# Kernel optimization log

Measured on AMD Instinct MI355X. Metric: run time of the kernel, lower is better.

The kernel has to match this reference:

```python
import jax, jax.numpy as jnp
import numpy as np
import math

RES = 320
DECIMATION = 4
M = RES * RES // DECIMATION  # 25600 trajectory points
OVERSAMP = 1.25
WIDTH = 4
BETA = math.pi * (((WIDTH / OVERSAMP) * (OVERSAMP - 0.5)) ** 2 - 0.8) ** 0.5
B = 16


def setup_inputs() -> dict:
    key = jax.random.key(0)
    k1, k2 = jax.random.split(key)
    k_space_input = jax.random.normal(k1, (B, 1, RES, RES, 2), dtype=jnp.float32)
    # learnable k-space trajectory, coords in [-RES/2, RES/2)
    trajectory = (jax.random.uniform(k2, (M, 2), dtype=jnp.float32) - 0.5) * RES
    return {"k_space_input": k_space_input, "trajectory": trajectory}


def _grid_sample_bilinear(img, traj):
    # img: [B, C, H, W]; traj: [M, 2] = (x, y) in [-res/2, res/2]
    # Matches torch grid_sample(align_corners=True, padding_mode='zeros')
    # after normalizing traj by (res/2).
    Bn, C, H, W = img.shape
    gx = traj[:, 0] / (W / 2)
    gy = traj[:, 1] / (H / 2)
    px = (gx + 1.0) * 0.5 * (W - 1)
    py = (gy + 1.0) * 0.5 * (H - 1)
    x0 = jnp.floor(px)
    y0 = jnp.floor(py)
    wx1 = px - x0
    wy1 = py - y0
    out = jnp.zeros((Bn, C, traj.shape[0]), img.dtype)
    for dy in (0, 1):
        for dx in (0, 1):
            xi = x0 + dx
            yi = y0 + dy
            w = (wx1 if dx else 1.0 - wx1) * (wy1 if dy else 1.0 - wy1)
            inb = (xi >= 0) & (xi < W) & (yi >= 0) & (yi < H)
            xc = jnp.clip(xi, 0, W - 1).astype(jnp.int32)
            yc = jnp.clip(yi, 0, H - 1).astype(jnp.int32)
            out = out + img[:, :, yc, xc] * (w * inb)[None, None, :]
    return out  # [B, C, M]


def _kb_weight(delta, half):
    # Kaiser-Bessel interpolation kernel (sigpy convention, 1/width factor per dim)
    x = delta / half
    t = jnp.maximum(1.0 - x * x, 0.0)
    return jnp.i0(BETA * jnp.sqrt(t)) / WIDTH


def _nufft_adjoint(y, coord, H, W):
    # y: [B, M] complex64; coord: [M,2], coord[:,0]->H axis, coord[:,1]->W axis
    osH = math.ceil(OVERSAMP * H)
    osW = math.ceil(OVERSAMP * W)
    scale = jnp.array([osH / H, osW / W], jnp.float32)
    shift = jnp.array([osH // 2, osW // 2], jnp.float32)
    c = coord * scale + shift  # scaled to oversampled-grid coords
    half = WIDTH / 2.0
    start = jnp.ceil(c - half)                       # [M,2]
    offs = jnp.arange(WIDTH, dtype=jnp.float32)
    idx = start[:, :, None] + offs                   # [M,2,WIDTH]
    w = _kb_weight(c[:, :, None] - idx, half)        # [M,2,WIDTH]
    iy = idx[:, 0].astype(jnp.int32) % osH           # [M,WIDTH]
    ix = idx[:, 1].astype(jnp.int32) % osW
    ww = w[:, 0, :, None] * w[:, 1, None, :]         # [M,WIDTH,WIDTH]
    flat = (iy[:, :, None] * osW + ix[:, None, :]).reshape(-1)  # [M*WIDTH^2]
    Bn = y.shape[0]
    contrib = (y[:, :, None, None] * ww[None]).reshape(Bn, -1)  # [B, M*WIDTH^2]
    grid = jnp.zeros((Bn, osH * osW), y.dtype).at[:, flat].add(contrib)
    grid = grid.reshape(Bn, osH, osW)
    # centered unnormalized-to-ortho IFFT (sigpy scaling)
    img = jnp.fft.fftshift(
        jnp.fft.ifft2(jnp.fft.ifftshift(grid, axes=(-2, -1)), axes=(-2, -1)),
        axes=(-2, -1))
    img = img * ((osH * osW) / math.sqrt(H * W))
    sy = osH // 2 - H // 2
    sx = osW // 2 - W // 2
    img = img[:, sy:sy + H, sx:sx + W]  # center crop

    def apod(n, os_n):
        a = jnp.sqrt(jnp.maximum(
            BETA ** 2 - (np.pi * WIDTH * (jnp.arange(n, dtype=jnp.float32) - n // 2) / os_n) ** 2,
            1e-12))
        return a / jnp.sinh(a)

    img = img * apod(H, osH)[:, None] * apod(W, osW)[None, :]
    return img  # [B, H, W] complex


def reference(k_space_input, trajectory):
    # [B,1,H,W,2] -> [B,2,H,W] (real/imag channels)
    ksp = jnp.transpose(k_space_input, (0, 1, 4, 2, 3))[:, 0]
    sub = _grid_sample_bilinear(ksp, trajectory)          # [B,2,M]
    y = (sub[:, 0] + 1j * sub[:, 1]).astype(jnp.complex64)
    img = _nufft_adjoint(y, trajectory, ksp.shape[-2], ksp.shape[-1])
    out = jnp.stack([img.real, img.imag], axis=1)          # [B,2,H,W]
    return out[:, None]                                    # [B,1,2,H,W]
```

## Files before the change

kernel.cpp:

```cpp
#include <hip/hip_runtime.h>

#define NPTS   25600
#define NB     16
#define NRES   320
#define OS     400
#define NCELL  (OS * OS)
#define CAP    16
#define MAXOVF 4096

#define NJ     8
#define FFTTH  512
#define LSTRV  404

#define BETA_F (3.14159265358979f * 2.22710574513201f)

__device__ __forceinline__ float bessel_i0f(float x) {
    float ax = fabsf(x);
    if (ax < 3.75f) {
        float t = (ax * ax) * (1.0f / 14.0625f);
        return 1.0f + t * (3.5156229f + t * (3.0899424f + t * (1.2067492f +
                     t * (0.2659732f + t * (0.0360768f + t * 0.0045813f)))));
    } else {
        float t = 3.75f / ax;
        return (expf(ax) * rsqrtf(ax)) *
               (0.39894228f + t * (0.01328592f + t * (0.00225319f + t * (-0.00157565f +
                t * (0.00916281f + t * (-0.02057706f + t * (0.02635537f +
                t * (-0.01647633f + t * 0.00392377f))))))));
    }
}

struct OvfEntry { int cell; int m; float w; float pad; };

__global__ __launch_bounds__(256)
void k_sample_taps(const float* __restrict__ ksp,
                   const float* __restrict__ traj,
                   float2* __restrict__ val,
                   int* __restrict__ cursor,
                   float2* __restrict__ entries,
                   int* __restrict__ ovf_cnt,
                   OvfEntry* __restrict__ ovf)
{
    int blk = blockIdx.x;
    if (blk < 1600) {
        int gid = blk * 256 + threadIdx.x;
        int b = gid & 15;
        int m = gid >> 4;

        float tx = traj[2 * m + 0];
        float ty = traj[2 * m + 1];

        float px = (tx * (1.0f / 160.0f) + 1.0f) * 0.5f * 319.0f;
        float py = (ty * (1.0f / 160.0f) + 1.0f) * 0.5f * 319.0f;
        float fx0 = floorf(px), fy0 = floorf(py);
        int x0 = (int)fx0, y0 = (int)fy0;
        float wx1 = px - fx0, wy1 = py - fy0;
        float wx0 = 1.0f - wx1, wy0 = 1.0f - wy1;
        x0 = min(max(x0, 0), NRES - 1);
        y0 = min(max(y0, 0), NRES - 1);
        int x1 = min(x0 + 1, NRES - 1);
        int y1 = min(y0 + 1, NRES - 1);

        const float2* base = (const float2*)ksp + (size_t)b * NRES * NRES;
        float2 v00 = base[y0 * NRES + x0];
        float2 v01 = base[y0 * NRES + x1];
        float2 v10 = base[y1 * NRES + x0];
        float2 v11 = base[y1 * NRES + x1];
        float sr = (v00.x * wx0 + v01.x * wx1) * wy0 + (v10.x * wx0 + v11.x * wx1) * wy1;
        float si = (v00.y * wx0 + v01.y * wx1) * wy0 + (v10.y * wx0 + v11.y * wx1) * wy1;

        val[gid] = make_float2(sr, si);
    } else {
        int m = (blk - 1600) * 256 + threadIdx.x;
        if (m >= NPTS) return;

        float tx = traj[2 * m + 0];
        float ty = traj[2 * m + 1];
        float c0 = tx * 1.25f + 200.0f;
        float c1 = ty * 1.25f + 200.0f;
        float s0 = ceilf(c0 - 2.0f);
        float s1 = ceilf(c1 - 2.0f);

        float w0[4], w1[4];
        int   i0[4], i1[4];
#pragma unroll
        for (int t = 0; t < 4; t++) {
            float id0 = s0 + (float)t;
            float d0 = (c0 - id0) * 0.5f;
            float t0 = fmaxf(1.0f - d0 * d0, 0.0f);
            w0[t] = bessel_i0f(BETA_F * sqrtf(t0)) * 0.25f;
            i0[t] = (((int)id0) + OS) % OS;

            float id1 = s1 + (float)t;
            float d1 = (c1 - id1) * 0.5f;
            float t1 = fmaxf(1.0f - d1 * d1, 0.0f);
            w1[t] = bessel_i0f(BETA_F * sqrtf(t1)) * 0.25f;
            i1[t] = (((int)id1) + OS) % OS;
        }

#pragma unroll
        for (int t0 = 0; t0 < 4; t0++) {
#pragma unroll
            for (int t1 = 0; t1 < 4; t1++) {
                int cell = i1[t1] * OS + i0[t0];
                float w = w0[t0] * w1[t1];
                int slot = atomicAdd(&cursor[cell], 1);
                if (slot < CAP) {
                    entries[(size_t)slot * NCELL + cell] = make_float2(__int_as_float(m), w);
                } else {
                    int oi = atomicAdd(ovf_cnt, 1);
                    if (oi < MAXOVF) { ovf[oi].cell = cell; ovf[oi].m = m; ovf[oi].w = w; }
                }
            }
        }
    }
}

__global__ __launch_bounds__(256)
void k_gather(const int* __restrict__ cursor,
              const float2* __restrict__ entries,
              const float4* __restrict__ val4,
              float2* __restrict__ grid,
              const int* __restrict__ ovf_cnt,
              const OvfEntry* __restrict__ ovf)
{
    int cell = blockIdx.x * blockDim.x + threadIdx.x;
    if (cell >= NCELL) return;
    int cnt_raw = cursor[cell];
    int cnt = min(cnt_raw, CAP);

    float4 acc[8];
#pragma unroll
    for (int q = 0; q < 8; q++) acc[q] = make_float4(0.f, 0.f, 0.f, 0.f);

    for (int k = 0; k < cnt; k++) {
        float2 e = entries[(size_t)k * NCELL + cell];
        int m = __float_as_int(e.x);
        float w = e.y;
        const float4* v = val4 + (size_t)m * 8;
#pragma unroll
        for (int q = 0; q < 8; q++) {
            float4 x = v[q];
            acc[q].x = fmaf(w, x.x, acc[q].x);
            acc[q].y = fmaf(w, x.y, acc[q].y);
            acc[q].z = fmaf(w, x.z, acc[q].z);
            acc[q].w = fmaf(w, x.w, acc[q].w);
        }
    }

    if (cnt_raw > CAP) {
        int n = min(*ovf_cnt, MAXOVF);
        for (int i = 0; i < n; i++) {
            if (ovf[i].cell != cell) continue;
            int m = ovf[i].m;
            float w = ovf[i].w;
            const float4* v = val4 + (size_t)m * 8;
#pragma unroll
            for (int q = 0; q < 8; q++) {
                float4 x = v[q];
                acc[q].x = fmaf(w, x.x, acc[q].x);
                acc[q].y = fmaf(w, x.y, acc[q].y);
                acc[q].z = fmaf(w, x.z, acc[q].z);
                acc[q].w = fmaf(w, x.w, acc[q].w);
            }
        }
    }

#pragma unroll
    for (int q = 0; q < 8; q++) {
        grid[(size_t)(2 * q + 0) * NCELL + cell] = make_float2(acc[q].x, acc[q].y);
        grid[(size_t)(2 * q + 1) * NCELL + cell] = make_float2(acc[q].z, acc[q].w);
    }
}


__device__ __forceinline__ float apodf(int i) {
    float t = (float)(i - 160) * 0.031415926535897932f;
    float a = sqrtf(fmaxf(BETA_F * BETA_F - t * t, 1e-12f));
    return a / sinhf(a);
}

__global__ __launch_bounds__(FFTTH)
void k_fft_pass_a(const float* __restrict__ grid, float* __restrict__ At)
{
    __shared__ float2 A[NJ * LSTRV];
    __shared__ float4 B4[NJ * 200];
    __shared__ float2 E20t[20];
    __shared__ float2 E400p[424];
    int tid = threadIdx.x;
    int b = blockIdx.y;
    int j0 = blockIdx.x * NJ;

    for (int t = tid; t < 400; t += FFTTH) {
        float sn, cs;
        sincosf((float)t * 0.015707963267948966f, &sn, &cs);
        E400p[t + (t >> 4)] = make_float2(cs, sn);
    }
    if (tid < 20) {
        float sn, cs;
        sincosf((float)tid * 0.3141592653589793f, &sn, &cs);
        E20t[tid] = make_float2(cs, sn);
    }
    const float4* g4 = (const float4*)(grid + ((size_t)b * NCELL + (size_t)j0 * OS) * 2);
    for (int o = tid; o < NJ * 200; o += FFTTH) {
        int r = o / 200, q = o - r * 200;
        *((float4*)&A[r * LSTRV] + q) = g4[r * 200 + q];
    }
    __syncthreads();

    for (int o = tid; o < NJ * 200; o += FFTTH) {
        int r = o / 200, rem = o - r * 200;
        int j = rem / 20, n2 = rem - j * 20;
        const float2* Al = &A[r * LSTRV];
        float4 outv;
        if (j == 0) {
            float2 a0 = Al[n2], a1 = Al[n2 + 200];
            outv = make_float4(a0.x, a0.y, a1.x, a1.y);
        } else {
            float2 a0 = Al[n2 + 20 * j], a1 = Al[n2 + 20 * (20 - j)];
            outv = make_float4(a0.x + a1.x, a0.y + a1.y, a0.x - a1.x, a0.y - a1.y);
        }
        B4[r * 200 + j * 20 + n2] = outv;
    }
    __syncthreads();

    for (int o = tid; o < NJ * 200; o += FFTTH) {
        int r = o / 200, rem = o - r * 200;
        int k1h = rem / 20, n2 = rem - k1h * 20;
        const float4* Bl = &B4[r * 200];
        float4 b0 = Bl[n2];
        float2* Ar_ = &A[r * LSTRV + 20 * n2];
        if (k1h == 0) {
            float b_r = b0.x + b0.z, b_i = b0.y + b0.w;
            float a0r = 0.f, a0i = 0.f, d0r = 0.f, d0i = 0.f;
#pragma unroll
            for (int j = 1; j <= 9; j++) {
                float4 P = Bl[j * 20 + n2];
                a0r += P.x; a0i += P.y;
                float sg = (j & 1) ? -1.f : 1.f;
                d0r = fmaf(sg, P.x, d0r); d0i = fmaf(sg, P.y, d0i);
            }
            Ar_[0] = make_float2(b_r + a0r, b_i + a0i);
            int ti = 10 * n2;
            float2 tw = E400p[ti + (ti >> 4)];
            float xr = b_r + d0r, xi = b_i + d0i;
            Ar_[10] = make_float2(xr * tw.x - xi * tw.y, xr * tw.y + xi * tw.x);
        } else {
            float sgn = (k1h & 1) ? -1.f : 1.f;
            float b_r = fmaf(sgn, b0.z, b0.x), b_i = fmaf(sgn, b0.w, b0.y);
            float2 ek = E20t[k1h];
            float c = ek.x, s = ek.y;
            float Asr = 0.f, Asi = 0.f, Bsr = 0.f, Bsi = 0.f;
#pragma unroll
            for (int j = 1; j <= 9; j++) {
                float4 P = Bl[j * 20 + n2];
                Asr = fmaf(c, P.x, Asr); Asi = fmaf(c, P.y, Asi);
                Bsr = fmaf(s, P.w, Bsr); Bsi = fmaf(s, P.z, Bsi);
                float cn = c * ek.x - s * ek.y;
                s = c * ek.y + s * ek.x;
                c = cn;
            }
            float x1r = b_r + Asr - Bsr, x1i = b_i + Asi + Bsi;
            float x2r = b_r + Asr + Bsr, x2i = b_i + Asi - Bsi;
            int t1 = n2 * k1h;
            int t2 = n2 * (20 - k1h);
            float2 tw1 = E400p[t1 + (t1 >> 4)];
            float2 tw2 = E400p[t2 + (t2 >> 4)];
            Ar_[k1h]      = make_float2(x1r * tw1.x - x1i * tw1.y, x1r * tw1.y + x1i * tw1.x);
            Ar_[20 - k1h] = make_float2(x2r * tw2.x - x2i * tw2.y, x2r * tw2.y + x2i * tw2.x);
        }
    }
    __syncthreads();

    for (int o = tid; o < NJ * 200; o += FFTTH) {
        int r = o / 200, rem = o - r * 200;
        int j = rem / 20, k1 = rem - j * 20;
        const float2* Sl = &A[r * LSTRV];
        float4 outv;
        if (j == 0) {
            float2 a0 = Sl[k1], a1 = Sl[200 + k1];
            outv = make_float4(a0.x, a0.y, a1.x, a1.y);
        } else {
            float2 a0 = Sl[20 * j + k1], a1 = Sl[20 * (20 - j) + k1];
            outv = make_float4(a0.x + a1.x, a0.y + a1.y, a0.x - a1.x, a0.y - a1.y);
        }
        B4[r * 200 + j * 20 + k1] = outv;
    }
    __syncthreads();

    for (int o = tid; o < NJ * 180; o += FFTTH) {
        int r = o / 180, rem = o - r * 180;
        int k2h = rem / 20, k1 = rem - k2h * 20;
        const float4* Bl = &B4[r * 200];
        float4 b0 = Bl[k1];
        float2* Ar_ = &A[r * LSTRV];
        if (k2h == 0) {
            float b_r = b0.x + b0.z, b_i = b0.y + b0.w;
            float a0r = 0.f, a0i = 0.f;
#pragma unroll
            for (int j = 1; j <= 9; j++) {
                float4 P = Bl[j * 20 + k1];
                a0r += P.x; a0i += P.y;
            }
            Ar_[k1] = make_float2(b_r + a0r, b_i + a0i);
        } else {
            float sgn = (k2h & 1) ? -1.f : 1.f;
            float b_r = fmaf(sgn, b0.z, b0.x), b_i = fmaf(sgn, b0.w, b0.y);
            float2 ek = E20t[k2h];
            float c = ek.x, s = ek.y;
            float Asr = 0.f, Asi = 0.f, Bsr = 0.f, Bsi = 0.f;
#pragma unroll
            for (int j = 1; j <= 9; j++) {
                float4 P = Bl[j * 20 + k1];
                Asr = fmaf(c, P.x, Asr); Asi = fmaf(c, P.y, Asi);
                Bsr = fmaf(s, P.w, Bsr); Bsi = fmaf(s, P.z, Bsi);
                float cn = c * ek.x - s * ek.y;
                s = c * ek.y + s * ek.x;
                c = cn;
            }
            if (k2h <= 7)
                Ar_[20 * k2h + k1] = make_float2(b_r + Asr - Bsr, b_i + Asi + Bsi);
            Ar_[320 - 20 * k2h + k1] = make_float2(b_r + Asr + Bsr, b_i + Asi - Bsi);
        }
    }
    __syncthreads();

    float2* At2 = (float2*)At;
    for (int o = tid; o < 320 * NJ; o += FFTTH) {
        int uc = o >> 3, r = o & 7;
        At2[((size_t)b * 320 + uc) * OS + j0 + r] = A[r * LSTRV + uc];
    }
}

__global__ __launch_bounds__(FFTTH)
void k_fft_pass_b(const float* __restrict__ At, float* __restrict__ out)
{
    __shared__ float2 A[NJ * LSTRV];
    __shared__ float4 B4[NJ * 200];
    __shared__ float2 E20t[20];
    __shared__ float2 E400p[424];
    __shared__ float apodT[320];
    int tid = threadIdx.x;
    int b = blockIdx.y;
    int uc0 = blockIdx.x * NJ;

    for (int t = tid; t < 400; t += FFTTH) {
        float sn, cs;
        sincosf((float)t * 0.015707963267948966f, &sn, &cs);
        E400p[t + (t >> 4)] = make_float2(cs, sn);
    }
    if (tid < 20) {
        float sn, cs;
        sincosf((float)tid * 0.3141592653589793f, &sn, &cs);
        E20t[tid] = make_float2(cs, sn);
    }
    for (int t = tid; t < 320; t += FFTTH) apodT[t] = apodf(t);

    const float4* a4 = (const float4*)(At + ((size_t)b * 320 + uc0) * OS * 2);
    for (int o = tid; o < NJ * 200; o += FFTTH) {
        int r = o / 200, q = o - r * 200;
        *((float4*)&A[r * LSTRV] + q) = a4[r * 200 + q];
    }
    __syncthreads();

    for (int o = tid; o < NJ * 200; o += FFTTH) {
        int r = o / 200, rem = o - r * 200;
        int j = rem / 20, n2 = rem - j * 20;
        const float2* Al = &A[r * LSTRV];
        float4 outv;
        if (j == 0) {
            float2 a0 = Al[n2], a1 = Al[n2 + 200];
            outv = make_float4(a0.x, a0.y, a1.x, a1.y);
        } else {
            float2 a0 = Al[n2 + 20 * j], a1 = Al[n2 + 20 * (20 - j)];
            outv = make_float4(a0.x + a1.x, a0.y + a1.y, a0.x - a1.x, a0.y - a1.y);
        }
        B4[r * 200 + j * 20 + n2] = outv;
    }
    __syncthreads();

    for (int o = tid; o < NJ * 200; o += FFTTH) {
        int r = o / 200, rem = o - r * 200;
        int k1h = rem / 20, n2 = rem - k1h * 20;
        const float4* Bl = &B4[r * 200];
        float4 b0 = Bl[n2];
        float2* Ar_ = &A[r * LSTRV + 20 * n2];
        if (k1h == 0) {
            float b_r = b0.x + b0.z, b_i = b0.y + b0.w;
            float a0r = 0.f, a0i = 0.f, d0r = 0.f, d0i = 0.f;
#pragma unroll
            for (int j = 1; j <= 9; j++) {
                float4 P = Bl[j * 20 + n2];
                a0r += P.x; a0i += P.y;
                float sg = (j & 1) ? -1.f : 1.f;
                d0r = fmaf(sg, P.x, d0r); d0i = fmaf(sg, P.y, d0i);
            }
            Ar_[0] = make_float2(b_r + a0r, b_i + a0i);
            int ti = 10 * n2;
            float2 tw = E400p[ti + (ti >> 4)];
            float xr = b_r + d0r, xi = b_i + d0i;
            Ar_[10] = make_float2(xr * tw.x - xi * tw.y, xr * tw.y + xi * tw.x);
        } else {
            float sgn = (k1h & 1) ? -1.f : 1.f;
            float b_r = fmaf(sgn, b0.z, b0.x), b_i = fmaf(sgn, b0.w, b0.y);
            float2 ek = E20t[k1h];
            float c = ek.x, s = ek.y;
            float Asr = 0.f, Asi = 0.f, Bsr = 0.f, Bsi = 0.f;
#pragma unroll
            for (int j = 1; j <= 9; j++) {
                float4 P = Bl[j * 20 + n2];
                Asr = fmaf(c, P.x, Asr); Asi = fmaf(c, P.y, Asi);
                Bsr = fmaf(s, P.w, Bsr); Bsi = fmaf(s, P.z, Bsi);
                float cn = c * ek.x - s * ek.y;
                s = c * ek.y + s * ek.x;
                c = cn;
            }
            float x1r = b_r + Asr - Bsr, x1i = b_i + Asi + Bsi;
            float x2r = b_r + Asr + Bsr, x2i = b_i + Asi - Bsi;
            int t1 = n2 * k1h;
            int t2 = n2 * (20 - k1h);
            float2 tw1 = E400p[t1 + (t1 >> 4)];
            float2 tw2 = E400p[t2 + (t2 >> 4)];
            Ar_[k1h]      = make_float2(x1r * tw1.x - x1i * tw1.y, x1r * tw1.y + x1i * tw1.x);
            Ar_[20 - k1h] = make_float2(x2r * tw2.x - x2i * tw2.y, x2r * tw2.y + x2i * tw2.x);
        }
    }
    __syncthreads();

    for (int o = tid; o < NJ * 200; o += FFTTH) {
        int r = o / 200, rem = o - r * 200;
        int j = rem / 20, k1 = rem - j * 20;
        const float2* Sl = &A[r * LSTRV];
        float4 outv;
        if (j == 0) {
            float2 a0 = Sl[k1], a1 = Sl[200 + k1];
            outv = make_float4(a0.x, a0.y, a1.x, a1.y);
        } else {
            float2 a0 = Sl[20 * j + k1], a1 = Sl[20 * (20 - j) + k1];
            outv = make_float4(a0.x + a1.x, a0.y + a1.y, a0.x - a1.x, a0.y - a1.y);
        }
        B4[r * 200 + j * 20 + k1] = outv;
    }
    __syncthreads();

    for (int o = tid; o < NJ * 180; o += FFTTH) {
        int r = o / 180, rem = o - r * 180;
        int k2h = rem / 20, k1 = rem - k2h * 20;
        const float4* Bl = &B4[r * 200];
        float4 b0 = Bl[k1];
        int y = uc0 + r + 160; if (y >= 320) y -= 320;
        float apy = (1.0f / 320.0f) * apodT[y];
        float* o0 = out + (((size_t)b * 2 + 0) * NRES + y) * NRES;
        float* o1 = out + (((size_t)b * 2 + 1) * NRES + y) * NRES;
        if (k2h == 0) {
            float b_r = b0.x + b0.z, b_i = b0.y + b0.w;
            float a0r = 0.f, a0i = 0.f;
#pragma unroll
            for (int j = 1; j <= 9; j++) {
                float4 P = Bl[j * 20 + k1];
                a0r += P.x; a0i += P.y;
            }
            int x = k1 + 160; if (x >= 320) x -= 320;
            float sg = ((x + y) & 1) ? -1.0f : 1.0f;
            float sc = sg * apy * apodT[x];
            o0[x] = (b_r + a0r) * sc;
            o1[x] = (b_i + a0i) * sc;
        } else {
            float sgn = (k2h & 1) ? -1.f : 1.f;
            float b_r = fmaf(sgn, b0.z, b0.x), b_i = fmaf(sgn, b0.w, b0.y);
            float2 ek = E20t[k2h];
            float c = ek.x, s = ek.y;
            float Asr = 0.f, Asi = 0.f, Bsr = 0.f, Bsi = 0.f;
#pragma unroll
            for (int j = 1; j <= 9; j++) {
                float4 P = Bl[j * 20 + k1];
                Asr = fmaf(c, P.x, Asr); Asi = fmaf(c, P.y, Asi);
                Bsr = fmaf(s, P.w, Bsr); Bsi = fmaf(s, P.z, Bsi);
                float cn = c * ek.x - s * ek.y;
                s = c * ek.y + s * ek.x;
                c = cn;
            }
            if (k2h <= 7) {
                int vc = 20 * k2h + k1;
                int x = vc + 160; if (x >= 320) x -= 320;
                float sg = ((x + y) & 1) ? -1.0f : 1.0f;
                float sc = sg * apy * apodT[x];
                o0[x] = (b_r + Asr - Bsr) * sc;
                o1[x] = (b_i + Asi + Bsi) * sc;
            }
            {
                int vc = 320 - 20 * k2h + k1;
                int x = vc + 160; if (x >= 320) x -= 320;
                float sg = ((x + y) & 1) ? -1.0f : 1.0f;
                float sc = sg * apy * apodT[x];
                o0[x] = (b_r + Asr + Bsr) * sc;
                o1[x] = (b_i + Asi - Bsi) * sc;
            }
        }
    }
}

extern "C" void kernel_launch(void* const* d_in, const int* in_sizes, int n_in,
                              void* d_out, int out_size, void* d_ws, size_t ws_size,
                              hipStream_t stream) {
    const float* ksp  = (const float*)d_in[0];
    const float* traj = (const float*)d_in[1];
    float* out = (float*)d_out;

    float* grid = (float*)d_ws;
    float* At   = grid + (size_t)NB * NCELL * 2;
    float2* entries = (float2*)(At + (size_t)NB * 320 * OS * 2);
    float2* val = (float2*)(entries + (size_t)CAP * NCELL);
    int* cursor  = (int*)(val + (size_t)NPTS * NB);
    int* ovf_cnt = cursor + NCELL;
    OvfEntry* ovf = (OvfEntry*)(ovf_cnt + 16);

    hipMemsetAsync(cursor, 0, (NCELL + 16) * sizeof(int), stream);

    k_sample_taps<<<dim3(1700), 256, 0, stream>>>(ksp, traj, val, cursor, entries, ovf_cnt, ovf);
    k_gather     <<<dim3((NCELL + 255) / 256), 256, 0, stream>>>(cursor, entries, (const float4*)val,
                                                                 (float2*)grid, ovf_cnt, ovf);
    k_fft_pass_a <<<dim3(OS / NJ, NB),  FFTTH, 0, stream>>>(grid, At);
    k_fft_pass_b <<<dim3(320 / NJ, NB), FFTTH, 0, stream>>>(At, out);
}
```

Baseline: 149.6 us.

## Fuse FFT butterfly pre-pass into DFT20 stage and double FFT block threads

Replaces the separate shared-memory B4 butterfly stage with an inline symmetric/antisymmetric pairing inside a new dft20_conj helper that reads A directly. This drops one shared buffer and two barrier-separated passes per FFT dimension, and the results are staged in registers so A can be updated in place. The FFT blocks grow to 1024 threads with a launch-bounds occupancy hint, and the twiddle and apodization table setup is spread across disjoint thread ranges. The cost is more shared loads per output in the DFT loops and heavier register pressure from the occupancy hint.

```diff
diff --git a/kernel.cpp b/kernel.cpp
--- a/kernel.cpp
+++ b/kernel.cpp
@@ -9,7 +9,7 @@
 #define MAXOVF 4096
 
 #define NJ     8
-#define FFTTH  512
+#define FFTTH  1024
 #define LSTRV  404
 
 #define BETA_F (3.14159265358979f * 2.22710574513201f)
@@ -172,6 +172,47 @@
     }
 }
 
+__device__ __forceinline__ void dft20_conj(const float2* __restrict__ Al, int off, int kh,
+                                           const float2* __restrict__ E20t,
+                                           float& y1r, float& y1i, float& y2r, float& y2i)
+{
+    float2 x0 = Al[off], x10 = Al[off + 200];
+    if (kh == 0) {
+        float br = x0.x + x10.x, bi = x0.y + x10.y;
+        float ar = 0.f, ai = 0.f, dr = 0.f, di = 0.f;
+#pragma unroll
+        for (int j = 1; j <= 9; j++) {
+            float2 xa = Al[off + 20 * j];
+            float2 xb = Al[off + 400 - 20 * j];
+            float pr = xa.x + xb.x, pi = xa.y + xb.y;
+            ar += pr; ai += pi;
+            float sg = (j & 1) ? -1.f : 1.f;
+            dr = fmaf(sg, pr, dr); di = fmaf(sg, pi, di);
+        }
+        y1r = br + ar; y1i = bi + ai;
+        y2r = br + dr; y2i = bi + di;
+    } else {
+        float sgn = (kh & 1) ? -1.f : 1.f;
+        float br = fmaf(sgn, x10.x, x0.x), bi = fmaf(sgn, x10.y, x0.y);
+        float2 ek = E20t[kh];
+        float c = ek.x, s = ek.y;
+        float Asr = 0.f, Asi = 0.f, Bsr = 0.f, Bsi = 0.f;
+#pragma unroll
+        for (int j = 1; j <= 9; j++) {
+            float2 xa = Al[off + 20 * j];
+            float2 xb = Al[off + 400 - 20 * j];
+            float pr = xa.x + xb.x, pi = xa.y + xb.y;
+            float mr = xa.x - xb.x, mi = xa.y - xb.y;
+            Asr = fmaf(c, pr, Asr); Asi = fmaf(c, pi, Asi);
+            Bsr = fmaf(s, mi, Bsr); Bsi = fmaf(s, mr, Bsi);
+            float cn = c * ek.x - s * ek.y;
+            s = c * ek.y + s * ek.x;
+            c = cn;
+        }
+        y1r = br + Asr - Bsr; y1i = bi + Asi + Bsi;
+        y2r = br + Asr + Bsr; y2i = bi + Asi - Bsi;
+    }
+}
 
 __device__ __forceinline__ float apodf(int i) {
     float t = (float)(i - 160) * 0.031415926535897932f;
@@ -179,147 +220,103 @@
     return a / sinhf(a);
 }
 
-__global__ __launch_bounds__(FFTTH)
+__global__ __launch_bounds__(FFTTH, 8)
 void k_fft_pass_a(const float* __restrict__ grid, float* __restrict__ At)
 {
-    __shared__ float2 A[NJ * LSTRV];
-    __shared__ float4 B4[NJ * 200];
+    __shared__ __align__(16) float2 A[NJ * LSTRV];
     __shared__ float2 E20t[20];
     __shared__ float2 E400p[424];
     int tid = threadIdx.x;
     int b = blockIdx.y;
     int j0 = blockIdx.x * NJ;
 
-    for (int t = tid; t < 400; t += FFTTH) {
+    if (tid < 400) {
         float sn, cs;
-        sincosf((float)t * 0.015707963267948966f, &sn, &cs);
-        E400p[t + (t >> 4)] = make_float2(cs, sn);
-    }
-    if (tid < 20) {
+        sincosf((float)tid * 0.015707963267948966f, &sn, &cs);
+        E400p[tid + (tid >> 4)] = make_float2(cs, sn);
+    } else if (tid >= 448 && tid < 468) {
+        int t = tid - 448;
         float sn, cs;
-        sincosf((float)tid * 0.3141592653589793f, &sn, &cs);
-        E20t[tid] = make_float2(cs, sn);
-    }
+        sincosf((float)t * 0.3141592653589793f, &sn, &cs);
+        E20t[t] = make_float2(cs, sn);
+    }
+
     const float4* g4 = (const float4*)(grid + ((size_t)b * NCELL + (size_t)j0 * OS) * 2);
+    float4* A4 = (float4*)A;
     for (int o = tid; o < NJ * 200; o += FFTTH) {
         int r = o / 200, q = o - r * 200;
-        *((float4*)&A[r * LSTRV] + q) = g4[r * 200 + q];
-    }
-    __syncthreads();
-
-    for (int o = tid; o < NJ * 200; o += FFTTH) {
-        int r = o / 200, rem = o - r * 200;
-        int j = rem / 20, n2 = rem - j * 20;
-        const float2* Al = &A[r * LSTRV];
-        float4 outv;
-        if (j == 0) {
-            float2 a0 = Al[n2], a1 = Al[n2 + 200];
-            outv = make_float4(a0.x, a0.y, a1.x, a1.y);
-        } else {
-            float2 a0 = Al[n2 + 20 * j], a1 = Al[n2 + 20 * (20 - j)];
-            outv = make_float4(a0.x + a1.x, a0.y + a1.y, a0.x - a1.x, a0.y - a1.y);
-        }
-        B4[r * 200 + j * 20 + n2] = outv;
-    }
-    __syncthreads();
-
-    for (int o = tid; o < NJ * 200; o += FFTTH) {
-        int r = o / 200, rem = o - r * 200;
-        int k1h = rem / 20, n2 = rem - k1h * 20;
-        const float4* Bl = &B4[r * 200];
-        float4 b0 = Bl[n2];
-        float2* Ar_ = &A[r * LSTRV + 20 * n2];
-        if (k1h == 0) {
-            float b_r = b0.x + b0.z, b_i = b0.y + b0.w;
-            float a0r = 0.f, a0i = 0.f, d0r = 0.f, d0i = 0.f;
-#pragma unroll
-            for (int j = 1; j <= 9; j++) {
-                float4 P = Bl[j * 20 + n2];
-                a0r += P.x; a0i += P.y;
-                float sg = (j & 1) ? -1.f : 1.f;
-                d0r = fmaf(sg, P.x, d0r); d0i = fmaf(sg, P.y, d0i);
-            }
-            Ar_[0] = make_float2(b_r + a0r, b_i + a0i);
-            int ti = 10 * n2;
-            float2 tw = E400p[ti + (ti >> 4)];
-            float xr = b_r + d0r, xi = b_i + d0i;
-            Ar_[10] = make_float2(xr * tw.x - xi * tw.y, xr * tw.y + xi * tw.x);
-        } else {
-            float sgn = (k1h & 1) ? -1.f : 1.f;
-            float b_r = fmaf(sgn, b0.z, b0.x), b_i = fmaf(sgn, b0.w, b0.y);
-            float2 ek = E20t[k1h];
-            float c = ek.x, s = ek.y;
-            float Asr = 0.f, Asi = 0.f, Bsr = 0.f, Bsi = 0.f;
-#pragma unroll
-            for (int j = 1; j <= 9; j++) {
-                float4 P = Bl[j * 20 + n2];
-                Asr = fmaf(c, P.x, Asr); Asi = fmaf(c, P.y, Asi);
-                Bsr = fmaf(s, P.w, Bsr); Bsi = fmaf(s, P.z, Bsi);
-                float cn = c * ek.x - s * ek.y;
-                s = c * ek.y + s * ek.x;
-                c = cn;
-            }
-            float x1r = b_r + Asr - Bsr, x1i = b_i + Asi + Bsi;
-            float x2r = b_r + Asr + Bsr, x2i = b_i + Asi - Bsi;
-            int t1 = n2 * k1h;
-            int t2 = n2 * (20 - k1h);
-            float2 tw1 = E400p[t1 + (t1 >> 4)];
-            float2 tw2 = E400p[t2 + (t2 >> 4)];
-            Ar_[k1h]      = make_float2(x1r * tw1.x - x1i * tw1.y, x1r * tw1.y + x1i * tw1.x);
-            Ar_[20 - k1h] = make_float2(x2r * tw2.x - x2i * tw2.y, x2r * tw2.y + x2i * tw2.x);
-        }
-    }
-    __syncthreads();
-
-    for (int o = tid; o < NJ * 200; o += FFTTH) {
-        int r = o / 200, rem = o - r * 200;
-        int j = rem / 20, k1 = rem - j * 20;
-        const float2* Sl = &A[r * LSTRV];
-        float4 outv;
-        if (j == 0) {
-            float2 a0 = Sl[k1], a1 = Sl[200 + k1];
-            outv = make_float4(a0.x, a0.y, a1.x, a1.y);
-        } else {
-            float2 a0 = Sl[20 * j + k1], a1 = Sl[20 * (20 - j) + k1];
-            outv = make_float4(a0.x + a1.x, a0.y + a1.y, a0.x - a1.x, a0.y - a1.y);
-        }
-        B4[r * 200 + j * 20 + k1] = outv;
-    }
-    __syncthreads();
-
-    for (int o = tid; o < NJ * 180; o += FFTTH) {
-        int r = o / 180, rem = o - r * 180;
-        int k2h = rem / 20, k1 = rem - k2h * 20;
-        const float4* Bl = &B4[r * 200];
-        float4 b0 = Bl[k1];
-        float2* Ar_ = &A[r * LSTRV];
-        if (k2h == 0) {
-            float b_r = b0.x + b0.z, b_i = b0.y + b0.w;
-            float a0r = 0.f, a0i = 0.f;
-#pragma unroll
-            for (int j = 1; j <= 9; j++) {
-                float4 P = Bl[j * 20 + k1];
-                a0r += P.x; a0i += P.y;
-            }
-            Ar_[k1] = make_float2(b_r + a0r, b_i + a0i);
-        } else {
-            float sgn = (k2h & 1) ? -1.f : 1.f;
-            float b_r = fmaf(sgn, b0.z, b0.x), b_i = fmaf(sgn, b0.w, b0.y);
-            float2 ek = E20t[k2h];
-            float c = ek.x, s = ek.y;
-            float Asr = 0.f, Asi = 0.f, Bsr = 0.f, Bsi = 0.f;
-#pragma unroll
-            for (int j = 1; j <= 9; j++) {
-                float4 P = Bl[j * 20 + k1];
-                Asr = fmaf(c, P.x, Asr); Asi = fmaf(c, P.y, Asi);
-                Bsr = fmaf(s, P.w, Bsr); Bsi = fmaf(s, P.z, Bsi);
-                float cn = c * ek.x - s * ek.y;
-                s = c * ek.y + s * ek.x;
-                c = cn;
-            }
-            if (k2h <= 7)
-                Ar_[20 * k2h + k1] = make_float2(b_r + Asr - Bsr, b_i + Asi + Bsi);
-            Ar_[320 - 20 * k2h + k1] = make_float2(b_r + Asr + Bsr, b_i + Asi - Bsi);
+        A4[r * (LSTRV / 2) + q] = g4[o];
+    }
+    __syncthreads();
+
+    float v1r[2], v1i[2], v2r[2], v2i[2];
+#pragma unroll
+    for (int it = 0; it < 2; it++) {
+        int o = tid + it * FFTTH;
+        if (o < NJ * 200) {
+            int r = o / 200, q = o - r * 200;
+            int kh = q / 20, n2 = q - kh * 20;
+            float y1r, y1i, y2r, y2i;
+            dft20_conj(&A[r * LSTRV], n2, kh, E20t, y1r, y1i, y2r, y2i);
+            if (kh == 0) {
+                v1r[it] = y1r; v1i[it] = y1i;
+                int ti = 10 * n2;
+                float2 tw = E400p[ti + (ti >> 4)];
+                v2r[it] = y2r * tw.x - y2i * tw.y; v2i[it] = y2r * tw.y + y2i * tw.x;
+            } else {
+                int t1 = n2 * kh, t2 = n2 * (20 - kh);
+                float2 w1 = E400p[t1 + (t1 >> 4)], w2 = E400p[t2 + (t2 >> 4)];
+                v1r[it] = y1r * w1.x - y1i * w1.y; v1i[it] = y1r * w1.y + y1i * w1.x;
+                v2r[it] = y2r * w2.x - y2i * w2.y; v2i[it] = y2r * w2.y + y2i * w2.x;
+            }
+        }
+    }
+    __syncthreads();
+#pragma unroll
+    for (int it = 0; it < 2; it++) {
+        int o = tid + it * FFTTH;
+        if (o < NJ * 200) {
+            int r = o / 200, q = o - r * 200;
+            int kh = q / 20, n2 = q - kh * 20;
+            float2* Al = &A[r * LSTRV + 20 * n2];
+            if (kh == 0) {
+                Al[0]  = make_float2(v1r[it], v1i[it]);
+                Al[10] = make_float2(v2r[it], v2i[it]);
+            } else {
+                Al[kh]      = make_float2(v1r[it], v1i[it]);
+                Al[20 - kh] = make_float2(v2r[it], v2i[it]);
+            }
+        }
+    }
+    __syncthreads();
+
+#pragma unroll
+    for (int it = 0; it < 2; it++) {
+        int o = tid + it * FFTTH;
+        if (o < NJ * 180) {
+            int r = o / 180, q = o - r * 180;
+            int k2h = q / 20, k1 = q - k2h * 20;
+            float y1r, y1i, y2r, y2i;
+            dft20_conj(&A[r * LSTRV], k1, k2h, E20t, y1r, y1i, y2r, y2i);
+            v1r[it] = y1r; v1i[it] = y1i;
+            v2r[it] = y2r; v2i[it] = y2i;
+        }
+    }
+    __syncthreads();
+#pragma unroll
+    for (int it = 0; it < 2; it++) {
+        int o = tid + it * FFTTH;
+        if (o < NJ * 180) {
+            int r = o / 180, q = o - r * 180;
+            int k2h = q / 20, k1 = q - k2h * 20;
+            float2* Al = &A[r * LSTRV];
+            if (k2h == 0) {
+                Al[k1] = make_float2(v1r[it], v1i[it]);
+            } else {
+                if (k2h <= 7)
+                    Al[20 * k2h + k1] = make_float2(v1r[it], v1i[it]);
+                Al[320 - 20 * k2h + k1] = make_float2(v2r[it], v2i[it]);
+            }
         }
     }
     __syncthreads();
@@ -331,11 +328,10 @@
     }
 }
 
-__global__ __launch_bounds__(FFTTH)
+__global__ __launch_bounds__(FFTTH, 8)
 void k_fft_pass_b(const float* __restrict__ At, float* __restrict__ out)
 {
-    __shared__ float2 A[NJ * LSTRV];
-    __shared__ float4 B4[NJ * 200];
+    __shared__ __align__(16) float2 A[NJ * LSTRV];
     __shared__ float2 E20t[20];
     __shared__ float2 E400p[424];
     __shared__ float apodT[320];
@@ -343,158 +339,95 @@
     int b = blockIdx.y;
     int uc0 = blockIdx.x * NJ;
 
-    for (int t = tid; t < 400; t += FFTTH) {
+    if (tid < 400) {
         float sn, cs;
-        sincosf((float)t * 0.015707963267948966f, &sn, &cs);
-        E400p[t + (t >> 4)] = make_float2(cs, sn);
-    }
-    if (tid < 20) {
+        sincosf((float)tid * 0.015707963267948966f, &sn, &cs);
+        E400p[tid + (tid >> 4)] = make_float2(cs, sn);
+    } else if (tid >= 448 && tid < 468) {
+        int t = tid - 448;
         float sn, cs;
-        sincosf((float)tid * 0.3141592653589793f, &sn, &cs);
-        E20t[tid] = make_float2(cs, sn);
-    }
-    for (int t = tid; t < 320; t += FFTTH) apodT[t] = apodf(t);
+        sincosf((float)t * 0.3141592653589793f, &sn, &cs);
+        E20t[t] = make_float2(cs, sn);
+    } else if (tid >= 512 && tid < 832) {
+        int t = tid - 512;
+        apodT[t] = apodf(t);
+    }
 
     const float4* a4 = (const float4*)(At + ((size_t)b * 320 + uc0) * OS * 2);
+    float4* A4 = (float4*)A;
     for (int o = tid; o < NJ * 200; o += FFTTH) {
         int r = o / 200, q = o - r * 200;
-        *((float4*)&A[r * LSTRV] + q) = a4[r * 200 + q];
-    }
-    __syncthreads();
-
-    for (int o = tid; o < NJ * 200; o += FFTTH) {
-        int r = o / 200, rem = o - r * 200;
-        int j = rem / 20, n2 = rem - j * 20;
-        const float2* Al = &A[r * LSTRV];
-        float4 outv;
-        if (j == 0) {
-            float2 a0 = Al[n2], a1 = Al[n2 + 200];
-            outv = make_float4(a0.x, a0.y, a1.x, a1.y);
-        } else {
-            float2 a0 = Al[n2 + 20 * j], a1 = Al[n2 + 20 * (20 - j)];
-            outv = make_float4(a0.x + a1.x, a0.y + a1.y, a0.x - a1.x, a0.y - a1.y);
-        }
-        B4[r * 200 + j * 20 + n2] = outv;
-    }
-    __syncthreads();
-
-    for (int o = tid; o < NJ * 200; o += FFTTH) {
-        int r = o / 200, rem = o - r * 200;
-        int k1h = rem / 20, n2 = rem - k1h * 20;
-        const float4* Bl = &B4[r * 200];
-        float4 b0 = Bl[n2];
-        float2* Ar_ = &A[r * LSTRV + 20 * n2];
-        if (k1h == 0) {
-            float b_r = b0.x + b0.z, b_i = b0.y + b0.w;
-            float a0r = 0.f, a0i = 0.f, d0r = 0.f, d0i = 0.f;
-#pragma unroll
-            for (int j = 1; j <= 9; j++) {
-                float4 P = Bl[j * 20 + n2];
-                a0r += P.x; a0i += P.y;
-                float sg = (j & 1) ? -1.f : 1.f;
-                d0r = fmaf(sg, P.x, d0r); d0i = fmaf(sg, P.y, d0i);
-            }
-            Ar_[0] = make_float2(b_r + a0r, b_i + a0i);
-            int ti = 10 * n2;
-            float2 tw = E400p[ti + (ti >> 4)];
-            float xr = b_r + d0r, xi = b_i + d0i;
-            Ar_[10] = make_float2(xr * tw.x - xi * tw.y, xr * tw.y + xi * tw.x);
-        } else {
-            float sgn = (k1h & 1) ? -1.f : 1.f;
-            float b_r = fmaf(sgn, b0.z, b0.x), b_i = fmaf(sgn, b0.w, b0.y);
-            float2 ek = E20t[k1h];
-            float c = ek.x, s = ek.y;
-            float Asr = 0.f, Asi = 0.f, Bsr = 0.f, Bsi = 0.f;
-#pragma unroll
-            for (int j = 1; j <= 9; j++) {
-                float4 P = Bl[j * 20 + n2];
-                Asr = fmaf(c, P.x, Asr); Asi = fmaf(c, P.y, Asi);
-                Bsr = fmaf(s, P.w, Bsr); Bsi = fmaf(s, P.z, Bsi);
-                float cn = c * ek.x - s * ek.y;
-                s = c * ek.y + s * ek.x;
-                c = cn;
-            }
-            float x1r = b_r + Asr - Bsr, x1i = b_i + Asi + Bsi;
-            float x2r = b_r + Asr + Bsr, x2i = b_i + Asi - Bsi;
-            int t1 = n2 * k1h;
-            int t2 = n2 * (20 - k1h);
-            float2 tw1 = E400p[t1 + (t1 >> 4)];
-            float2 tw2 = E400p[t2 + (t2 >> 4)];
-            Ar_[k1h]      = make_float2(x1r * tw1.x - x1i * tw1.y, x1r * tw1.y + x1i * tw1.x);
-            Ar_[20 - k1h] = make_float2(x2r * tw2.x - x2i * tw2.y, x2r * tw2.y + x2i * tw2.x);
-        }
-    }
-    __syncthreads();
-
-    for (int o = tid; o < NJ * 200; o += FFTTH) {
-        int r = o / 200, rem = o - r * 200;
-        int j = rem / 20, k1 = rem - j * 20;
-        const float2* Sl = &A[r * LSTRV];
-        float4 outv;
-        if (j == 0) {
-            float2 a0 = Sl[k1], a1 = Sl[200 + k1];
-            outv = make_float4(a0.x, a0.y, a1.x, a1.y);
-        } else {
-            float2 a0 = Sl[20 * j + k1], a1 = Sl[20 * (20 - j) + k1];
-            outv = make_float4(a0.x + a1.x, a0.y + a1.y, a0.x - a1.x, a0.y - a1.y);
-        }
-        B4[r * 200 + j * 20 + k1] = outv;
+        A4[r * (LSTRV / 2) + q] = a4[o];
+    }
+    __syncthreads();
+
+    float v1r[2], v1i[2], v2r[2], v2i[2];
+#pragma unroll
+    for (int it = 0; it < 2; it++) {
+        int o = tid + it * FFTTH;
+        if (o < NJ * 200) {
+            int r = o / 200, q = o - r * 200;
+            int kh = q / 20, n2 = q - kh * 20;
+            float y1r, y1i, y2r, y2i;
+            dft20_conj(&A[r * LSTRV], n2, kh, E20t, y1r, y1i, y2r, y2i);
+            if (kh == 0) {
+                v1r[it] = y1r; v1i[it] = y1i;
+                int ti = 10 * n2;
+                float2 tw = E400p[ti + (ti >> 4)];
+                v2r[it] = y2r * tw.x - y2i * tw.y; v2i[it] = y2r * tw.y + y2i * tw.x;
+            } else {
+                int t1 = n2 * kh, t2 = n2 * (20 - kh);
+                float2 w1 = E400p[t1 + (t1 >> 4)], w2 = E400p[t2 + (t2 >> 4)];
+                v1r[it] = y1r * w1.x - y1i * w1.y; v1i[it] = y1r * w1.y + y1i * w1.x;
+                v2r[it] = y2r * w2.x - y2i * w2.y; v2i[it] = y2r * w2.y + y2i * w2.x;
+            }
+        }
+    }
+    __syncthreads();
+#pragma unroll
+    for (int it = 0; it < 2; it++) {
+        int o = tid + it * FFTTH;
+        if (o < NJ * 200) {
+            int r = o / 200, q = o - r * 200;
+            int kh = q / 20, n2 = q - kh * 20;
+            float2* Al = &A[r * LSTRV + 20 * n2];
+            if (kh == 0) {
+                Al[0]  = make_float2(v1r[it], v1i[it]);
+                Al[10] = make_float2(v2r[it], v2i[it]);
+            } else {
+                Al[kh]      = make_float2(v1r[it], v1i[it]);
+                Al[20 - kh] = make_float2(v2r[it], v2i[it]);
+            }
+        }
     }
     __syncthreads();
 
     for (int o = tid; o < NJ * 180; o += FFTTH) {
-        int r = o / 180, rem = o - r * 180;
-        int k2h = rem / 20, k1 = rem - k2h * 20;
-        const float4* Bl = &B4[r * 200];
-        float4 b0 = Bl[k1];
+        int r = o / 180, q = o - r * 180;
+        int k2h = q / 20, k1 = q - k2h * 20;
+        float y1r, y1i, y2r, y2i;
+        dft20_conj(&A[r * LSTRV], k1, k2h, E20t, y1r, y1i, y2r, y2i);
+
         int y = uc0 + r + 160; if (y >= 320) y -= 320;
         float apy = (1.0f / 320.0f) * apodT[y];
         float* o0 = out + (((size_t)b * 2 + 0) * NRES + y) * NRES;
         float* o1 = out + (((size_t)b * 2 + 1) * NRES + y) * NRES;
-        if (k2h == 0) {
-            float b_r = b0.x + b0.z, b_i = b0.y + b0.w;
-            float a0r = 0.f, a0i = 0.f;
-#pragma unroll
-            for (int j = 1; j <= 9; j++) {
-                float4 P = Bl[j * 20 + k1];
-                a0r += P.x; a0i += P.y;
-            }
-            int x = k1 + 160; if (x >= 320) x -= 320;
+
+        if (k2h <= 7) {
+            int vc = 20 * k2h + k1;
+            int x = vc + 160; if (x >= 320) x -= 320;
             float sg = ((x + y) & 1) ? -1.0f : 1.0f;
             float sc = sg * apy * apodT[x];
-            o0[x] = (b_r + a0r) * sc;
-            o1[x] = (b_i + a0i) * sc;
-        } else {
-            float sgn = (k2h & 1) ? -1.f : 1.f;
-            float b_r = fmaf(sgn, b0.z, b0.x), b_i = fmaf(sgn, b0.w, b0.y);
-            float2 ek = E20t[k2h];
-            float c = ek.x, s = ek.y;
-            float Asr = 0.f, Asi = 0.f, Bsr = 0.f, Bsi = 0.f;
-#pragma unroll
-            for (int j = 1; j <= 9; j++) {
-                float4 P = Bl[j * 20 + k1];
-                Asr = fmaf(c, P.x, Asr); Asi = fmaf(c, P.y, Asi);
-                Bsr = fmaf(s, P.w, Bsr); Bsi = fmaf(s, P.z, Bsi);
-                float cn = c * ek.x - s * ek.y;
-                s = c * ek.y + s * ek.x;
-                c = cn;
-            }
-            if (k2h <= 7) {
-                int vc = 20 * k2h + k1;
-                int x = vc + 160; if (x >= 320) x -= 320;
-                float sg = ((x + y) & 1) ? -1.0f : 1.0f;
-                float sc = sg * apy * apodT[x];
-                o0[x] = (b_r + Asr - Bsr) * sc;
-                o1[x] = (b_i + Asi + Bsi) * sc;
-            }
-            {
-                int vc = 320 - 20 * k2h + k1;
-                int x = vc + 160; if (x >= 320) x -= 320;
-                float sg = ((x + y) & 1) ? -1.0f : 1.0f;
-                float sc = sg * apy * apodT[x];
-                o0[x] = (b_r + Asr + Bsr) * sc;
-                o1[x] = (b_i + Asi - Bsi) * sc;
-            }
+            o0[x] = y1r * sc;
+            o1[x] = y1i * sc;
+        }
+        if (k2h >= 1) {
+            int vc = 320 - 20 * k2h + k1;
+            int x = vc + 160; if (x >= 320) x -= 320;
+            float sg = ((x + y) & 1) ? -1.0f : 1.0f;
+            float sc = sg * apy * apodT[x];
+            o0[x] = y2r * sc;
+            o1[x] = y2i * sc;
         }
     }
 }
```

Result: no change. 151.1 us (+1.0%).
